# Optimization experiments

Hardware: AMD Instinct MI355X
Metric: run time of the kernel (lower is better)

Reference implementation:

```python
import jax, jax.numpy as jnp
import numpy as np

B, S, D = 4, 2048, 2048
NH, NKV = 16, 4
HD = D // NH  # 128


def setup_inputs() -> dict:
    key = jax.random.key(0)
    ks = jax.random.split(key, 6)
    sd = 1.0 / np.sqrt(D)
    return {
        "x": jax.random.normal(ks[0], (B, S, D), jnp.float32),
        "cos": jax.random.normal(ks[1], (1, 1, S, HD), jnp.float32),
        "sin": jax.random.normal(ks[2], (1, 1, S, HD), jnp.float32),
        "wq_w": jax.random.normal(ks[3], (D, D), jnp.float32) * sd,
        "wk_w": jax.random.normal(ks[4], (NKV * HD, D), jnp.float32) * sd,
        "wv_w": jax.random.normal(ks[5], (NKV * HD, D), jnp.float32) * sd,
        "start_pos": 0,
    }


def _rotate_half(t):
    h = t.shape[-1] // 2
    return jnp.concatenate([-t[..., h:], t[..., :h]], axis=-1)


def reference(x, cos, sin, wq_w, wk_w, wv_w, start_pos):
    b, s, d = x.shape
    n_rep = NH // NKV
    q = (x @ wq_w.T).reshape(b, s, NH, HD).transpose(0, 2, 1, 3)      # [b,H,s,hd]
    k = (x @ wk_w.T).reshape(b, s, NKV, HD).transpose(0, 2, 1, 3)     # [b,Hk,s,hd]
    v = (x @ wv_w.T).reshape(b, s, NKV, HD).transpose(0, 2, 1, 3)
    # rotary
    q = q * cos + _rotate_half(q) * sin
    k = k * cos + _rotate_half(k) * sin
    # repeat_kv
    k = jnp.repeat(k, n_rep, axis=1)   # [b,H,s,hd]
    v = jnp.repeat(v, n_rep, axis=1)
    scores = jnp.einsum("bhqd,bhkd->bhqk", q, k) / jnp.sqrt(jnp.float32(HD))
    causal = jnp.tril(jnp.ones((s, s), dtype=bool))
    scores = jnp.where(causal, scores, jnp.float32(-jnp.inf))
    w = jax.nn.softmax(scores, axis=-1)
    out = jnp.einsum("bhqk,bhkd->bhqd", w, v)
    return out.transpose(0, 2, 1, 3).reshape(b, s, d)
```

## Files before the change

### kernel.cpp

```cpp
#include <hip/hip_runtime.h>
#include <hip/hip_bf16.h>
#include <math.h>

#define B_ 4
#define S_ 2048
#define D_ 2048
#define NH_ 16
#define NKV_ 4
#define HD_ 128

typedef short bf16x8 __attribute__((ext_vector_type(8)));
typedef float f32x4 __attribute__((ext_vector_type(4)));
typedef unsigned u32x4 __attribute__((ext_vector_type(4)));
typedef __hip_bfloat16 bf16;

#define ASYNC_CP16(gp, lp)                                                    \
  __builtin_amdgcn_global_load_lds(                                           \
      (const __attribute__((address_space(1))) unsigned int*)(gp),            \
      (__attribute__((address_space(3))) unsigned int*)(lp), 16, 0, 0)

__global__ __launch_bounds__(256) void cvt_kernel(const float* __restrict__ in,
                                                  bf16* __restrict__ out, int n4) {
  int i = blockIdx.x * 256 + threadIdx.x;
  if (i >= n4) return;
  float4 v = ((const float4*)in)[i];
  union { ushort4 u; bf16 h[4]; } o;
  o.h[0] = __float2bfloat16(v.x);
  o.h[1] = __float2bfloat16(v.y);
  o.h[2] = __float2bfloat16(v.z);
  o.h[3] = __float2bfloat16(v.w);
  ((ushort4*)out)[i] = o.u;
}

__global__ __launch_bounds__(256) void gemm_qkv(
    const bf16* __restrict__ A, const bf16* __restrict__ W,
    bf16* __restrict__ qr, bf16* __restrict__ kr, bf16* __restrict__ vlin,
    const float* __restrict__ cosp, const float* __restrict__ sinp,
    float qscale) {
  __shared__ __align__(16) bf16 As[128 * 64];
  __shared__ __align__(16) bf16 Bs[128 * 64];
  const int tid = threadIdx.x;
  const int lane = tid & 63, wave = tid >> 6;
  const int wm = (wave & 1) * 64, wn = (wave >> 1) * 64;
  const int m0 = blockIdx.x * 128;
  const int hblk = blockIdx.y;
  const int n0 = hblk * 128;
  const int quad = lane >> 4, c = lane & 15;
  const int K = 2048;

  f32x4 acc[4][4] = {};

  const int sr = lane >> 3;
  const int sg = lane & 7;
  const int gc = (sg ^ sr) * 8;
  const bf16* Ap = A + (size_t)(m0 + wave * 32 + sr) * K + gc;
  const bf16* Bp = W + (size_t)(n0 + wave * 32 + sr) * K + gc;

  for (int kb = 0; kb < K; kb += 64) {
    __syncthreads();
#pragma unroll
    for (int i = 0; i < 4; i++) {
      ASYNC_CP16(Ap + (size_t)(i * 8) * K + kb, &As[(wave * 32 + i * 8) * 64]);
      ASYNC_CP16(Bp + (size_t)(i * 8) * K + kb, &Bs[(wave * 32 + i * 8) * 64]);
    }
    __syncthreads();
#pragma unroll
    for (int kk = 0; kk < 2; kk++) {
      const int slot = ((kk * 4 + quad) ^ (c & 7)) * 8;
      bf16x8 af[4], bfr[4];
#pragma unroll
      for (int t = 0; t < 4; t++) {
        af[t]  = *(const bf16x8*)(&As[(wm + t * 16 + c) * 64 + slot]);
        bfr[t] = *(const bf16x8*)(&Bs[(wn + t * 16 + c) * 64 + slot]);
      }
#pragma unroll
      for (int mt = 0; mt < 4; mt++)
#pragma unroll
        for (int nt = 0; nt < 4; nt++)
          acc[mt][nt] = __builtin_amdgcn_mfma_f32_16x16x32_bf16(
              af[mt], bfr[nt], acc[mt][nt], 0, 0, 0);
    }
  }

  if (hblk >= 20) {
    const int colb = (hblk - 20) * 128 + wn;
#pragma unroll
    for (int mt = 0; mt < 4; mt++)
#pragma unroll
      for (int reg = 0; reg < 4; reg++) {
        int m = m0 + wm + mt * 16 + quad * 4 + reg;
        bf16* row = vlin + (size_t)m * (NKV_ * HD_) + colb;
#pragma unroll
        for (int nt = 0; nt < 4; nt++)
          row[nt * 16 + c] = __float2bfloat16(acc[mt][nt][reg]);
      }
  } else {
    float* Sc = (float*)As;
    __syncthreads();
    if (wave >= 2) {
#pragma unroll
      for (int mt = 0; mt < 4; mt++)
#pragma unroll
        for (int reg = 0; reg < 4; reg++) {
          int lr = wm + mt * 16 + quad * 4 + reg;
#pragma unroll
          for (int nt = 0; nt < 4; nt++)
            Sc[lr * 64 + nt * 16 + c] = acc[mt][nt][reg];
        }
    }
    __syncthreads();
    if (wave < 2) {
      const float scale = (hblk < 16) ? qscale : 1.0f;
#pragma unroll
      for (int mt = 0; mt < 4; mt++)
#pragma unroll
        for (int reg = 0; reg < 4; reg++) {
          int lr = wm + mt * 16 + quad * 4 + reg;
          int m = m0 + lr;
          int b = m >> 11, s = m & 2047;
          const float* cr = cosp + s * HD_;
          const float* sn = sinp + s * HD_;
          bf16* orow = (hblk < 16)
              ? qr + ((size_t)(b * NH_ + hblk) * S_ + s) * HD_
              : kr + ((size_t)(b * NKV_ + (hblk - 16)) * S_ + s) * HD_;
#pragma unroll
          for (int nt = 0; nt < 4; nt++) {
            int d1 = nt * 16 + c, d2 = d1 + 64;
            float q1 = acc[mt][nt][reg];
            float q2 = Sc[lr * 64 + d1];
            float o1 = (q1 * cr[d1] - q2 * sn[d1]) * scale;
            float o2 = (q2 * cr[d2] + q1 * sn[d2]) * scale;
            orow[d1] = __float2bfloat16(o1);
            orow[d2] = __float2bfloat16(o2);
          }
        }
    }
  }
}

__global__ __launch_bounds__(256) void v_transpose(const bf16* __restrict__ in,
                                                   int instride,
                                                   bf16* __restrict__ out) {
  __shared__ __align__(16) bf16 tile[64][HD_ + 8];
  int bidx = blockIdx.x;
  int st = bidx & 31;
  int kv = (bidx >> 5) & 3;
  int b = bidx >> 7;
  int s0 = st * 64;
  int t = threadIdx.x;
  {
    int row = t >> 2;
    int colb = (t & 3) * 32;
#pragma unroll
    for (int i = 0; i < 4; i++) {
      int col = colb + i * 8;
      *(uint4*)(&tile[row][col]) = *(const uint4*)(
          &in[(size_t)(b * S_ + s0 + row) * instride + kv * HD_ + col]);
    }
  }
  __syncthreads();
  int sl = t & 63, hb = t >> 6;
#pragma unroll
  for (int i = 0; i < 32; i++) {
    int hd = i * 4 + hb;
    out[((size_t)(b * NKV_ + kv) * HD_ + hd) * S_ + s0 + sl] = tile[sl][hd];
  }
}

__device__ __forceinline__ void attn_step(
    const bf16* __restrict__ Ks, const bf16* __restrict__ Vs,
    bf16* __restrict__ Psw, const bf16x8* qf, f32x4* o,
    float& m_i, float& l_i, bool diag, int kb, int qbase, int quad, int c) {
  f32x4 sacc[4] = {};
#pragma unroll
  for (int kt = 0; kt < 4; kt++) {
    const int slot = ((kt * 4 + quad) ^ (c & 7)) * 8;
#pragma unroll
    for (int mt = 0; mt < 4; mt++) {
      bf16x8 kf = *(const bf16x8*)(&Ks[(mt * 16 + c) * 128 + slot]);
      sacc[mt] = __builtin_amdgcn_mfma_f32_16x16x32_bf16(kf, qf[kt], sacc[mt], 0, 0, 0);
    }
  }
  if (diag) {
    const int qg = qbase + c;
#pragma unroll
    for (int mt = 0; mt < 4; mt++)
#pragma unroll
      for (int r = 0; r < 4; r++)
        if (kb + mt * 16 + quad * 4 + r > qg) sacc[mt][r] = -INFINITY;
  }
  f32x4 mx4 = __builtin_elementwise_max(
      __builtin_elementwise_max(sacc[0], sacc[1]),
      __builtin_elementwise_max(sacc[2], sacc[3]));
  float mx = fmaxf(fmaxf(mx4[0], mx4[1]), fmaxf(mx4[2], mx4[3]));
  mx = fmaxf(mx, __shfl_xor(mx, 16, 64));
  mx = fmaxf(mx, __shfl_xor(mx, 32, 64));
  const float mnew = fmaxf(m_i, mx);
  const float alpha = exp2f(m_i - mnew);
  m_i = mnew;
  const f32x4 mn4 = {mnew, mnew, mnew, mnew};
  f32x4 rs4 = {0.f, 0.f, 0.f, 0.f};
#pragma unroll
  for (int mt = 0; mt < 4; mt++) {
    f32x4 e = sacc[mt] - mn4;
    f32x4 p;
    p[0] = exp2f(e[0]); p[1] = exp2f(e[1]);
    p[2] = exp2f(e[2]); p[3] = exp2f(e[3]);
    rs4 += p;
    u32x4 u = __builtin_bit_cast(u32x4, p) + 0x8000u;
    uint2 pk;
    pk.x = __builtin_amdgcn_perm(u[1], u[0], 0x07060302u);
    pk.y = __builtin_amdgcn_perm(u[3], u[2], 0x07060302u);
    const int pslot = mt * 2 + (quad >> 1);
    *(uint2*)(&Psw[c * 64 + ((pslot ^ (c & 7)) << 3) + (quad & 1) * 4]) = pk;
  }
  float rs = (rs4[0] + rs4[1]) + (rs4[2] + rs4[3]);
  rs += __shfl_xor(rs, 16, 64);
  rs += __shfl_xor(rs, 32, 64);
  l_i = l_i * alpha + rs;
  if (__any(alpha != 1.0f)) {
    f32x4 av;
    av[0] = __shfl(alpha, quad * 4 + 0, 64);
    av[1] = __shfl(alpha, quad * 4 + 1, 64);
    av[2] = __shfl(alpha, quad * 4 + 2, 64);
    av[3] = __shfl(alpha, quad * 4 + 3, 64);
#pragma unroll
    for (int nt = 0; nt < 8; nt++) o[nt] *= av;
  }
#pragma unroll
  for (int kk = 0; kk < 2; kk++) {
    bf16x8 pf = *(const bf16x8*)(&Psw[c * 64 + (((kk * 4 + quad) ^ (c & 7)) << 3)]);
    const int slot = ((kk * 4 + quad) ^ (c & 7)) * 8;
#pragma unroll
    for (int nt = 0; nt < 8; nt++) {
      bf16x8 vf = *(const bf16x8*)(&Vs[(nt * 16 + c) * 64 + slot]);
      o[nt] = __builtin_amdgcn_mfma_f32_16x16x32_bf16(pf, vf, o[nt], 0, 0, 0);
    }
  }
}

__global__ __launch_bounds__(256, 4) void attn_kernel(const bf16* __restrict__ Q,
                                                      const bf16* __restrict__ Kr,
                                                      const bf16* __restrict__ Vt,
                                                      float* __restrict__ O) {
  __shared__ __align__(16) bf16 Ks[64 * 128];
  __shared__ __align__(16) bf16 Vs[128 * 64];
  __shared__ __align__(16) bf16 Ps[4][16 * 64];

  const int tid = threadIdx.x, lane = tid & 63, wave = tid >> 6;
  const int quad = lane >> 4, c = lane & 15;
  const int j = blockIdx.x;
  const int bh = blockIdx.y;
  const int b = bh >> 4, h = bh & 15, kv = h >> 2;
  bf16* Psw = &Ps[wave][0];

  const bf16* kbase = Kr + (size_t)(b * NKV_ + kv) * S_ * HD_;
  const bf16* vbase = Vt + (size_t)(b * NKV_ + kv) * HD_ * S_;

  int koff[4], voff;
  {
    const int kl = lane >> 4;
    const int ks = lane & 15;
#pragma unroll
    for (int i = 0; i < 4; i++) {
      int r = wave * 16 + i * 4 + kl;
      koff[i] = r * HD_ + ((ks ^ (r & 7)) * 8);
    }
    const int vl = lane >> 3;
    const int vs = lane & 7;
    voff = (wave * 32 + vl) * S_ + ((vs ^ (vl & 7)) * 8);
  }

#pragma unroll 1
  for (int pass = 0; pass < 2; ++pass) {
    const int qt = pass ? (31 - j) : j;
    const int q0 = qt * 64;
    const int qb = q0 + wave * 16;

    bf16x8 qf[4];
    {
      const bf16* qp = Q + ((size_t)(b * NH_ + h) * S_ + qb + c) * HD_;
#pragma unroll
      for (int kt = 0; kt < 4; kt++)
        qf[kt] = *(const bf16x8*)(qp + kt * 32 + quad * 8);
    }
    f32x4 o_acc[8] = {};
    float m_i = -INFINITY, l_i = 0.f;

#pragma unroll 1
    for (int it = 0; it <= qt; ++it) {
      const int kb = it * 64;
      __syncthreads();
#pragma unroll
      for (int i = 0; i < 4; i++) {
        ASYNC_CP16(kbase + (size_t)kb * HD_ + koff[i], &Ks[(wave * 16 + i * 4) * 128]);
        ASYNC_CP16(vbase + kb + voff + (size_t)(i * 8) * S_, &Vs[(wave * 32 + i * 8) * 64]);
      }
      __syncthreads();
      attn_step(Ks, Vs, Psw, qf, o_acc, m_i, l_i, it == qt, kb, qb, quad, c);
    }

    float inv[4];
#pragma unroll
    for (int r = 0; r < 4; r++) inv[r] = 1.0f / __shfl(l_i, quad * 4 + r, 64);
    float* obase = O + (size_t)b * S_ * D_ + (size_t)h * HD_;
#pragma unroll
    for (int nt = 0; nt < 8; nt++)
#pragma unroll
      for (int r = 0; r < 4; r++)
        obase[(size_t)(qb + quad * 4 + r) * D_ + nt * 16 + c] = o_acc[nt][r] * inv[r];
  }
}

extern "C" void kernel_launch(void* const* d_in, const int* in_sizes, int n_in,
                              void* d_out, int out_size, void* d_ws, size_t ws_size,
                              hipStream_t stream) {
  const float* x    = (const float*)d_in[0];
  const float* cosp = (const float*)d_in[1];
  const float* sinp = (const float*)d_in[2];
  const float* wq   = (const float*)d_in[3];
  const float* wk   = (const float*)d_in[4];
  const float* wv   = (const float*)d_in[5];
  float* out = (float*)d_out;

  char* ws = (char*)d_ws;
  const size_t MB = 1024 * 1024;
  bf16* xb    = (bf16*)(ws + 0);
  bf16* wqkvb = (bf16*)(ws + 32 * MB);
  bf16* qr    = (bf16*)(ws + 44 * MB);
  bf16* kr    = (bf16*)(ws + 76 * MB);
  bf16* vlin  = (bf16*)(ws + 84 * MB);
  bf16* vt    = (bf16*)(ws + 92 * MB);

  cvt_kernel<<<16384, 256, 0, stream>>>(x, xb, 4194304);
  cvt_kernel<<<4096, 256, 0, stream>>>(wq, wqkvb, 1048576);
  cvt_kernel<<<1024, 256, 0, stream>>>(wk, wqkvb + 4194304, 262144);
  cvt_kernel<<<1024, 256, 0, stream>>>(wv, wqkvb + 5242880, 262144);

  const float qscale = 1.4426950408889634f / 11.313708498984761f;
  gemm_qkv<<<dim3(64, 24), 256, 0, stream>>>(xb, wqkvb, qr, kr, vlin,
                                             cosp, sinp, qscale);

  v_transpose<<<512, 256, 0, stream>>>(vlin, NKV_ * HD_, vt);

  attn_kernel<<<dim3(16, 64), 256, 0, stream>>>(qr, kr, vt, out);
}
```

Measured before the change: 388.1 us.

## Fuse V transpose into QKV GEMM epilogue and use 128-row attention tiles

The V projection epilogue now writes its output already transposed ([b,kv,hd,s]) with packed 4-element stores, so the separate v_transpose kernel and its intermediate buffer are removed. The attention kernel moves to 512 threads (8 waves) covering 128 query rows per block, so each K/V tile loaded into shared memory is reused by twice as many queries. Each wave now issues half as many async copies per tile. The diagonal-masking condition is now decided per wave, and the larger block may lower occupancy under the new launch bounds.

```diff
diff --git a/kernel.cpp b/kernel.cpp
--- a/kernel.cpp
+++ b/kernel.cpp
@@ -18,6 +18,12 @@
   __builtin_amdgcn_global_load_lds(                                           \
       (const __attribute__((address_space(1))) unsigned int*)(gp),            \
       (__attribute__((address_space(3))) unsigned int*)(lp), 16, 0, 0)
+
+__device__ __forceinline__ short f2b(float f) {
+  union { bf16 h; short s; } u;
+  u.h = __float2bfloat16(f);
+  return u.s;
+}
 
 __global__ __launch_bounds__(256) void cvt_kernel(const float* __restrict__ in,
                                                   bf16* __restrict__ out, int n4) {
@@ -34,7 +40,7 @@
 
 __global__ __launch_bounds__(256) void gemm_qkv(
     const bf16* __restrict__ A, const bf16* __restrict__ W,
-    bf16* __restrict__ qr, bf16* __restrict__ kr, bf16* __restrict__ vlin,
+    bf16* __restrict__ qr, bf16* __restrict__ kr, bf16* __restrict__ vt,
     const float* __restrict__ cosp, const float* __restrict__ sinp,
     float qscale) {
   __shared__ __align__(16) bf16 As[128 * 64];
@@ -83,17 +89,23 @@
   }
 
   if (hblk >= 20) {
-    const int colb = (hblk - 20) * 128 + wn;
-#pragma unroll
-    for (int mt = 0; mt < 4; mt++)
-#pragma unroll
-      for (int reg = 0; reg < 4; reg++) {
-        int m = m0 + wm + mt * 16 + quad * 4 + reg;
-        bf16* row = vlin + (size_t)m * (NKV_ * HD_) + colb;
-#pragma unroll
-        for (int nt = 0; nt < 4; nt++)
-          row[nt * 16 + c] = __float2bfloat16(acc[mt][nt][reg]);
+    const int kv = hblk - 20;
+#pragma unroll
+    for (int mt = 0; mt < 4; mt++) {
+      const int m = m0 + wm + mt * 16 + quad * 4;
+      const int b = m >> 11, s0 = m & 2047;
+      bf16* obase = vt + ((size_t)(b * NKV_ + kv) * HD_) * S_ + s0;
+#pragma unroll
+      for (int nt = 0; nt < 4; nt++) {
+        const int hd = wn + nt * 16 + c;
+        short4 pk;
+        pk.x = f2b(acc[mt][nt][0]);
+        pk.y = f2b(acc[mt][nt][1]);
+        pk.z = f2b(acc[mt][nt][2]);
+        pk.w = f2b(acc[mt][nt][3]);
+        *(short4*)(obase + (size_t)hd * S_) = pk;
       }
+    }
   } else {
     float* Sc = (float*)As;
     __syncthreads();
@@ -135,35 +147,6 @@
           }
         }
     }
-  }
-}
-
-__global__ __launch_bounds__(256) void v_transpose(const bf16* __restrict__ in,
-                                                   int instride,
-                                                   bf16* __restrict__ out) {
-  __shared__ __align__(16) bf16 tile[64][HD_ + 8];
-  int bidx = blockIdx.x;
-  int st = bidx & 31;
-  int kv = (bidx >> 5) & 3;
-  int b = bidx >> 7;
-  int s0 = st * 64;
-  int t = threadIdx.x;
-  {
-    int row = t >> 2;
-    int colb = (t & 3) * 32;
-#pragma unroll
-    for (int i = 0; i < 4; i++) {
-      int col = colb + i * 8;
-      *(uint4*)(&tile[row][col]) = *(const uint4*)(
-          &in[(size_t)(b * S_ + s0 + row) * instride + kv * HD_ + col]);
-    }
-  }
-  __syncthreads();
-  int sl = t & 63, hb = t >> 6;
-#pragma unroll
-  for (int i = 0; i < 32; i++) {
-    int hd = i * 4 + hb;
-    out[((size_t)(b * NKV_ + kv) * HD_ + hd) * S_ + s0 + sl] = tile[sl][hd];
   }
 }
 
@@ -239,13 +222,13 @@
   }
 }
 
-__global__ __launch_bounds__(256, 4) void attn_kernel(const bf16* __restrict__ Q,
+__global__ __launch_bounds__(512, 6) void attn_kernel(const bf16* __restrict__ Q,
                                                       const bf16* __restrict__ Kr,
                                                       const bf16* __restrict__ Vt,
                                                       float* __restrict__ O) {
   __shared__ __align__(16) bf16 Ks[64 * 128];
   __shared__ __align__(16) bf16 Vs[128 * 64];
-  __shared__ __align__(16) bf16 Ps[4][16 * 64];
+  __shared__ __align__(16) bf16 Ps[8][16 * 64];
 
   const int tid = threadIdx.x, lane = tid & 63, wave = tid >> 6;
   const int quad = lane >> 4, c = lane & 15;
@@ -257,24 +240,28 @@
   const bf16* kbase = Kr + (size_t)(b * NKV_ + kv) * S_ * HD_;
   const bf16* vbase = Vt + (size_t)(b * NKV_ + kv) * HD_ * S_;
 
-  int koff[4], voff;
+  int koff[2], voff[2];
   {
     const int kl = lane >> 4;
     const int ks = lane & 15;
 #pragma unroll
-    for (int i = 0; i < 4; i++) {
-      int r = wave * 16 + i * 4 + kl;
+    for (int i = 0; i < 2; i++) {
+      int r = wave * 8 + i * 4 + kl;
       koff[i] = r * HD_ + ((ks ^ (r & 7)) * 8);
     }
     const int vl = lane >> 3;
     const int vs = lane & 7;
-    voff = (wave * 32 + vl) * S_ + ((vs ^ (vl & 7)) * 8);
+#pragma unroll
+    for (int i = 0; i < 2; i++) {
+      int r = wave * 16 + i * 8 + vl;
+      voff[i] = r * S_ + ((vs ^ (vl & 7)) * 8);
+    }
   }
 
 #pragma unroll 1
   for (int pass = 0; pass < 2; ++pass) {
-    const int qt = pass ? (31 - j) : j;
-    const int q0 = qt * 64;
+    const int qt = pass ? (15 - j) : j;
+    const int q0 = qt * 128;
     const int qb = q0 + wave * 16;
 
     bf16x8 qf[4];
@@ -287,17 +274,18 @@
     f32x4 o_acc[8] = {};
     float m_i = -INFINITY, l_i = 0.f;
 
+    const int nsteps = 2 * qt + 2;
 #pragma unroll 1
-    for (int it = 0; it <= qt; ++it) {
+    for (int it = 0; it < nsteps; ++it) {
       const int kb = it * 64;
       __syncthreads();
 #pragma unroll
-      for (int i = 0; i < 4; i++) {
-        ASYNC_CP16(kbase + (size_t)kb * HD_ + koff[i], &Ks[(wave * 16 + i * 4) * 128]);
-        ASYNC_CP16(vbase + kb + voff + (size_t)(i * 8) * S_, &Vs[(wave * 32 + i * 8) * 64]);
+      for (int i = 0; i < 2; i++) {
+        ASYNC_CP16(kbase + (size_t)kb * HD_ + koff[i], &Ks[(wave * 8 + i * 4) * 128]);
+        ASYNC_CP16(vbase + kb + voff[i], &Vs[(wave * 16 + i * 8) * 64]);
       }
       __syncthreads();
-      attn_step(Ks, Vs, Psw, qf, o_acc, m_i, l_i, it == qt, kb, qb, quad, c);
+      attn_step(Ks, Vs, Psw, qf, o_acc, m_i, l_i, kb + 63 > qb, kb, qb, quad, c);
     }
 
     float inv[4];
@@ -329,8 +317,7 @@
   bf16* wqkvb = (bf16*)(ws + 32 * MB);
   bf16* qr    = (bf16*)(ws + 44 * MB);
   bf16* kr    = (bf16*)(ws + 76 * MB);
-  bf16* vlin  = (bf16*)(ws + 84 * MB);
-  bf16* vt    = (bf16*)(ws + 92 * MB);
+  bf16* vt    = (bf16*)(ws + 84 * MB);
 
   cvt_kernel<<<16384, 256, 0, stream>>>(x, xb, 4194304);
   cvt_kernel<<<4096, 256, 0, stream>>>(wq, wqkvb, 1048576);
@@ -338,10 +325,8 @@
   cvt_kernel<<<1024, 256, 0, stream>>>(wv, wqkvb + 5242880, 262144);
 
   const float qscale = 1.4426950408889634f / 11.313708498984761f;
-  gemm_qkv<<<dim3(64, 24), 256, 0, stream>>>(xb, wqkvb, qr, kr, vlin,
+  gemm_qkv<<<dim3(64, 24), 256, 0, stream>>>(xb, wqkvb, qr, kr, vt,
                                              cosp, sinp, qscale);
 
-  v_transpose<<<512, 256, 0, stream>>>(vlin, NKV_ * HD_, vt);
-
-  attn_kernel<<<dim3(16, 64), 256, 0, stream>>>(qr, kr, vt, out);
-}
+  attn_kernel<<<dim3(8, 64), 512, 0, stream>>>(qr, kr, vt, out);
+}
```

Result: slower. 499.7 us (+28.8%).
